# Kernel tuning notes

Hardware: AMD Instinct MI355X
Metric: run time of the kernel (lower is better)

The kernel has to match this reference:

```python
import jax, jax.numpy as jnp
import numpy as np

M, K, N = 4096, 4096, 11008

def setup_inputs() -> dict:
    key = jax.random.key(0)
    k1, k2, k3, k4 = jax.random.split(key, 4)
    x = jax.random.normal(k1, (M, K), dtype=jnp.float32)
    weight = jax.random.randint(k2, (K, N), 0, 127, dtype=jnp.int32)
    antiquant_scale = jax.random.uniform(k3, (N,), dtype=jnp.float32)
    antiquant_offset = jax.random.normal(k4, (N,), dtype=jnp.float32)
    return {"x": x, "weight": weight, "antiquant_scale": antiquant_scale, "antiquant_offset": antiquant_offset}

def reference(x, weight, antiquant_scale, antiquant_offset):
    # Dequantize: (w + offset) * scale, per output channel (broadcast over K)
    dequantized_weight = (weight.astype(jnp.float32) + antiquant_offset) * antiquant_scale  # [K, N]
    return jnp.matmul(x, dequantized_weight)  # [M, N]
```

## Files before the change

kernel.cpp:

```cpp
#include <hip/hip_runtime.h>
#include <hip/hip_bf16.h>
#include <stdint.h>

#define M_DIM 4096
#define K_DIM 4096
#define N_DIM 11008
#define BKT 64
#define NT (K_DIM / BKT)
#define GRID_MN 688
#define NBLK_M 16

typedef __attribute__((ext_vector_type(8))) short short8;
typedef __attribute__((ext_vector_type(4))) float floatx4;

__device__ __forceinline__ short f2bf(float f) {
  union { float f; uint32_t u; } c; c.f = f;
  uint32_t u = c.u;
  u += 0x7FFFu + ((u >> 16) & 1u);
  return (short)(u >> 16);
}

__device__ __forceinline__ void gload_lds16(const void* g, void* l) {
  __builtin_amdgcn_global_load_lds(
      (const __attribute__((address_space(1))) unsigned int*)g,
      (__attribute__((address_space(3))) unsigned int*)l, 16, 0, 0);
}

__global__ __launch_bounds__(256) void convert_x_kernel(const float* __restrict__ x,
                                                        short* __restrict__ xb,
                                                        float* __restrict__ rowsum) {
  const int m = blockIdx.x;
  const int t = threadIdx.x;
  const float* row = x + (size_t)m * K_DIM + t * 16;
  short* orow = xb + (size_t)m * K_DIM + t * 16;
  float4 v0 = *(const float4*)(row + 0);
  float4 v1 = *(const float4*)(row + 4);
  float4 v2 = *(const float4*)(row + 8);
  float4 v3 = *(const float4*)(row + 12);
  float sum = v0.x + v0.y + v0.z + v0.w
            + v1.x + v1.y + v1.z + v1.w
            + v2.x + v2.y + v2.z + v2.w
            + v3.x + v3.y + v3.z + v3.w;
  short8 o0, o1;
  o0[0] = f2bf(v0.x); o0[1] = f2bf(v0.y); o0[2] = f2bf(v0.z); o0[3] = f2bf(v0.w);
  o0[4] = f2bf(v1.x); o0[5] = f2bf(v1.y); o0[6] = f2bf(v1.z); o0[7] = f2bf(v1.w);
  o1[0] = f2bf(v2.x); o1[1] = f2bf(v2.y); o1[2] = f2bf(v2.z); o1[3] = f2bf(v2.w);
  o1[4] = f2bf(v3.x); o1[5] = f2bf(v3.y); o1[6] = f2bf(v3.z); o1[7] = f2bf(v3.w);
  *(short8*)(orow) = o0;
  *(short8*)(orow + 8) = o1;
  #pragma unroll
  for (int off = 32; off > 0; off >>= 1) sum += __shfl_down(sum, off);
  __shared__ float part[4];
  if ((t & 63) == 0) part[t >> 6] = sum;
  __syncthreads();
  if (t == 0) rowsum[m] = part[0] + part[1] + part[2] + part[3];
}

__global__ __launch_bounds__(256) void convert_w_kernel(const int* __restrict__ w,
                                                        short* __restrict__ wt) {
  __shared__ short tile[64][72];
  const int bk = blockIdx.x * 64;
  const int bn = blockIdx.y * 64;
  const int t = threadIdx.x;
  const int kr = t >> 2;
  const int c0 = (t & 3) * 16;
  const int* src = w + (size_t)(bk + kr) * N_DIM + bn + c0;
  int4 a = *(const int4*)(src + 0);
  int4 b = *(const int4*)(src + 4);
  int4 c = *(const int4*)(src + 8);
  int4 d = *(const int4*)(src + 12);
  short* dst = &tile[kr][c0];
  dst[0]  = f2bf((float)a.x); dst[1]  = f2bf((float)a.y);
  dst[2]  = f2bf((float)a.z); dst[3]  = f2bf((float)a.w);
  dst[4]  = f2bf((float)b.x); dst[5]  = f2bf((float)b.y);
  dst[6]  = f2bf((float)b.z); dst[7]  = f2bf((float)b.w);
  dst[8]  = f2bf((float)c.x); dst[9]  = f2bf((float)c.y);
  dst[10] = f2bf((float)c.z); dst[11] = f2bf((float)c.w);
  dst[12] = f2bf((float)d.x); dst[13] = f2bf((float)d.y);
  dst[14] = f2bf((float)d.z); dst[15] = f2bf((float)d.w);
  __syncthreads();
  const int nr = t >> 2;
  short8 o0, o1;
  #pragma unroll
  for (int j = 0; j < 8; ++j) o0[j] = tile[c0 + j][nr];
  #pragma unroll
  for (int j = 0; j < 8; ++j) o1[j] = tile[c0 + 8 + j][nr];
  short* odst = wt + (size_t)(bn + nr) * K_DIM + bk + c0;
  *(short8*)(odst) = o0;
  *(short8*)(odst + 8) = o1;
}

__global__ __launch_bounds__(512, 2) void gemm_kernel(const short* __restrict__ xb,
                                                      const short* __restrict__ wt,
                                                      const float* __restrict__ scale,
                                                      const float* __restrict__ offset,
                                                      const float* __restrict__ rowsum,
                                                      float* __restrict__ out) {
  __shared__ short lds[2][4][8192];
  const int tid = threadIdx.x;
  const int bid = blockIdx.x;
  const int wg = (bid & 7) * (GRID_MN / 8) + (bid >> 3);
  const int bm = (wg % NBLK_M) * 256;
  const int bn = (wg / NBLK_M) * 256;

  const int wid = tid >> 6;
  const int lane = tid & 63;
  const int wr = wid >> 2;
  const int wc = wid & 3;
  const int hb = wc >> 1;
  const int lr = lane & 15;
  const int lg = lane >> 4;
  const int swz = lr & 7;
  const int gk0 = (lg ^ swz) * 8;
  const int gk1 = ((lg ^ 4) ^ swz) * 8;
  const int brow = (wc & 1) * 64 + lr;

  const int srow = tid >> 3;
  const int glog = (tid & 7) ^ (srow & 7);

  const size_t toff = (size_t)srow * K_DIM + glog * 8;
  const short* pA0 = xb + (size_t)bm * K_DIM + toff;
  const short* pA1 = xb + ((size_t)bm + 128) * K_DIM + toff;
  const short* pB0 = wt + (size_t)bn * K_DIM + toff;
  const short* pB1 = wt + ((size_t)bn + 128) * K_DIM + toff;

  auto stage2 = [&](const short* p, short* region) {
    gload_lds16(p, (char*)region + tid * 16);
    gload_lds16(p + (size_t)64 * K_DIM, (char*)region + (tid + 512) * 16);
  };

  floatx4 acc[8][4];
  const floatx4 zero = {0.f, 0.f, 0.f, 0.f};
  #pragma unroll
  for (int i = 0; i < 8; ++i)
    #pragma unroll
    for (int j = 0; j < 4; ++j) acc[i][j] = zero;

  stage2(pA0, &lds[0][0][0]);
  stage2(pA1, &lds[0][1][0]);
  stage2(pB0, &lds[0][2][0]);
  stage2(pB1, &lds[0][3][0]);
  stage2(pB0 + BKT, &lds[1][2][0]);
  stage2(pA0 + BKT, &lds[1][0][0]);
  stage2(pB1 + BKT, &lds[1][3][0]);
  asm volatile("s_waitcnt vmcnt(6)" ::: "memory");
  __builtin_amdgcn_s_barrier();
  pA1 += BKT;
  pA0 += 2 * BKT;
  pB0 += 2 * BKT;
  pB1 += 2 * BKT;

  const short* const AsB[2] = {&lds[0][wr][0], &lds[1][wr][0]};
  const short* const BsB[2] = {&lds[0][2 + hb][0], &lds[1][2 + hb][0]};

  short8 a03[4][2], a47[4][2], b0[2][2], b1[2][2];
  {
    const short* As = AsB[0];
    #pragma unroll
    for (int mf = 0; mf < 4; ++mf) {
      const short* p = As + (mf * 16 + lr) * 64;
      a03[mf][0] = *(const short8*)(p + gk0);
      a03[mf][1] = *(const short8*)(p + gk1);
    }
    const short* Bsp = BsB[0];
    #pragma unroll
    for (int nf = 0; nf < 2; ++nf) {
      const short* p = Bsp + (brow + nf * 16) * 64;
      b0[nf][0] = *(const short8*)(p + gk0);
      b0[nf][1] = *(const short8*)(p + gk1);
    }
  }

#define STEP_BODY(G, GN)                                                       \
  {                                                                            \
    const short* As = AsB[G];                                                  \
    const short* Bs = BsB[G];                                                  \
                    \
    _Pragma("unroll")                                                          \
    for (int mf = 0; mf < 4; ++mf) {                                           \
      const short* p = As + ((mf + 4) * 16 + lr) * 64;                         \
      a47[mf][0] = *(const short8*)(p + gk0);                                  \
      a47[mf][1] = *(const short8*)(p + gk1);                                  \
    }                                                                          \
    asm volatile("s_waitcnt lgkmcnt(8)" ::: "memory");                         \
    __builtin_amdgcn_s_barrier();                                              \
    if (u + 1 < NT) stage2(pA1, &lds[GN][1][0]);                               \
    pA1 += BKT;                                                                \
    __builtin_amdgcn_s_setprio(1);                                             \
    _Pragma("unroll")                                                          \
    for (int mf = 0; mf < 4; ++mf)                                             \
      _Pragma("unroll")                                                        \
      for (int nf = 0; nf < 2; ++nf) {                                         \
        acc[mf][nf] = __builtin_amdgcn_mfma_f32_16x16x32_bf16(a03[mf][0], b0[nf][0], acc[mf][nf], 0, 0, 0); \
        acc[mf][nf] = __builtin_amdgcn_mfma_f32_16x16x32_bf16(a03[mf][1], b0[nf][1], acc[mf][nf], 0, 0, 0); \
      }                                                                        \
    __builtin_amdgcn_s_setprio(0);                                             \
                      \
    _Pragma("unroll")                                                          \
    for (int nf = 0; nf < 2; ++nf) {                                           \
      const short* q = Bs + (brow + (nf + 2) * 16) * 64;                       \
      b1[nf][0] = *(const short8*)(q + gk0);                                   \
      b1[nf][1] = *(const short8*)(q + gk1);                                   \
    }                                                                          \
    asm volatile("s_waitcnt lgkmcnt(4)" ::: "memory");                         \
    __builtin_amdgcn_s_barrier();                                              \
    if (u + 2 < NT) stage2(pA0, &lds[G][0][0]);                                \
    pA0 += BKT;                                                                \
    __builtin_amdgcn_s_setprio(1);                                             \
    _Pragma("unroll")                                                          \
    for (int mf = 0; mf < 4; ++mf)                                             \
      _Pragma("unroll")                                                        \
      for (int nf = 0; nf < 2; ++nf) {                                         \
        acc[mf + 4][nf] = __builtin_amdgcn_mfma_f32_16x16x32_bf16(a47[mf][0], b0[nf][0], acc[mf + 4][nf], 0, 0, 0); \
        acc[mf + 4][nf] = __builtin_amdgcn_mfma_f32_16x16x32_bf16(a47[mf][1], b0[nf][1], acc[mf + 4][nf], 0, 0, 0); \
      }                                                                        \
    __builtin_amdgcn_s_setprio(0);                                             \
                                  \
    asm volatile("s_waitcnt lgkmcnt(0)" ::: "memory");                         \
    __builtin_amdgcn_s_barrier();                                              \
    if (u + 2 < NT) stage2(pB0, &lds[G][2][0]);                                \
    pB0 += BKT;                                                                \
    __builtin_amdgcn_s_setprio(1);                                             \
    _Pragma("unroll")                                                          \
    for (int mf = 0; mf < 4; ++mf)                                             \
      _Pragma("unroll")                                                        \
      for (int nf = 0; nf < 2; ++nf) {                                         \
        acc[mf][nf + 2] = __builtin_amdgcn_mfma_f32_16x16x32_bf16(a03[mf][0], b1[nf][0], acc[mf][nf + 2], 0, 0, 0); \
        acc[mf][nf + 2] = __builtin_amdgcn_mfma_f32_16x16x32_bf16(a03[mf][1], b1[nf][1], acc[mf][nf + 2], 0, 0, 0); \
      }                                                                        \
    __builtin_amdgcn_s_setprio(0);                                             \
      \
    if (u + 2 < NT) {                                                          \
      stage2(pB1, &lds[G][3][0]);                                              \
      asm volatile("s_waitcnt vmcnt(6)" ::: "memory");                         \
    } else {                                                                   \
      asm volatile("s_waitcnt vmcnt(0)" ::: "memory");                         \
    }                                                                          \
    pB1 += BKT;                                                                \
    __builtin_amdgcn_s_barrier();                                              \
    if (u + 1 < NT) {                                                          \
      const short* An = AsB[GN];                                               \
      const short* Bn = BsB[GN];                                               \
      _Pragma("unroll")                                                        \
      for (int mf = 0; mf < 4; ++mf) {                                         \
        const short* p = An + (mf * 16 + lr) * 64;                             \
        a03[mf][0] = *(const short8*)(p + gk0);                                \
        a03[mf][1] = *(const short8*)(p + gk1);                                \
      }                                                                        \
      _Pragma("unroll")                                                        \
      for (int nf = 0; nf < 2; ++nf) {                                         \
        const short* p = Bn + (brow + nf * 16) * 64;                           \
        b0[nf][0] = *(const short8*)(p + gk0);                                 \
        b0[nf][1] = *(const short8*)(p + gk1);                                 \
      }                                                                        \
    }                                                                          \
    __builtin_amdgcn_s_setprio(1);                                             \
    _Pragma("unroll")                                                          \
    for (int mf = 0; mf < 4; ++mf)                                             \
      _Pragma("unroll")                                                        \
      for (int nf = 0; nf < 2; ++nf) {                                         \
        acc[mf + 4][nf + 2] = __builtin_amdgcn_mfma_f32_16x16x32_bf16(a47[mf][0], b1[nf][0], acc[mf + 4][nf + 2], 0, 0, 0); \
        acc[mf + 4][nf + 2] = __builtin_amdgcn_mfma_f32_16x16x32_bf16(a47[mf][1], b1[nf][1], acc[mf + 4][nf + 2], 0, 0, 0); \
      }                                                                        \
    __builtin_amdgcn_s_setprio(0);                                             \
  }

  for (int u = 0; u < NT; u += 2) {
    STEP_BODY(0, 1)
    ++u;
    STEP_BODY(1, 0)
    --u;
  }
#undef STEP_BODY

  const int orow0 = bm + wr * 128 + lg * 4;
  const int ocol0 = bn + wc * 64 + lr;
  float4 rsv[8];
  #pragma unroll
  for (int amf = 0; amf < 8; ++amf)
    rsv[amf] = *(const float4*)&rowsum[orow0 + amf * 16];
  #pragma unroll
  for (int anf = 0; anf < 4; ++anf) {
    const int n = ocol0 + anf * 16;
    const float sc = scale[n];
    const float of = offset[n];
    #pragma unroll
    for (int amf = 0; amf < 8; ++amf) {
      const int mbase = orow0 + amf * 16;
      const float4 rv = rsv[amf];
      out[(size_t)(mbase + 0) * N_DIM + n] = (acc[amf][anf][0] + of * rv.x) * sc;
      out[(size_t)(mbase + 1) * N_DIM + n] = (acc[amf][anf][1] + of * rv.y) * sc;
      out[(size_t)(mbase + 2) * N_DIM + n] = (acc[amf][anf][2] + of * rv.z) * sc;
      out[(size_t)(mbase + 3) * N_DIM + n] = (acc[amf][anf][3] + of * rv.w) * sc;
    }
  }
}

__global__ __launch_bounds__(256) void fallback_gemm(const float* __restrict__ x,
                                                     const int* __restrict__ w,
                                                     const float* __restrict__ scale,
                                                     const float* __restrict__ offset,
                                                     float* __restrict__ out) {
  __shared__ float xs[32][33];
  __shared__ float bs[32][33];
  const int bm = blockIdx.y * 32, bn = blockIdx.x * 32;
  const int t = threadIdx.x;
  const int tm = t >> 5, tn = t & 31;
  float acc[4] = {0.f, 0.f, 0.f, 0.f};
  for (int k0 = 0; k0 < K_DIM; k0 += 32) {
    #pragma unroll
    for (int i = 0; i < 4; ++i) {
      int idx = t + i * 256; int r = idx >> 5, c = idx & 31;
      xs[r][c] = x[(size_t)(bm + r) * K_DIM + k0 + c];
      bs[r][c] = ((float)w[(size_t)(k0 + r) * N_DIM + bn + c] + offset[bn + c]) * scale[bn + c];
    }
    __syncthreads();
    #pragma unroll 8
    for (int kk = 0; kk < 32; ++kk) {
      float wv = bs[kk][tn];
      #pragma unroll
      for (int i = 0; i < 4; ++i) acc[i] += xs[tm + 8 * i][kk] * wv;
    }
    __syncthreads();
  }
  #pragma unroll
  for (int i = 0; i < 4; ++i)
    out[(size_t)(bm + tm + 8 * i) * N_DIM + bn + tn] = acc[i];
}

extern "C" void kernel_launch(void* const* d_in, const int* in_sizes, int n_in,
                              void* d_out, int out_size, void* d_ws, size_t ws_size,
                              hipStream_t stream) {
  const float* x      = (const float*)d_in[0];
  const int*   w      = (const int*)d_in[1];
  const float* scale  = (const float*)d_in[2];
  const float* offset = (const float*)d_in[3];
  float* out = (float*)d_out;

  const size_t xb_bytes = (size_t)M_DIM * K_DIM * 2;
  const size_t wt_bytes = (size_t)N_DIM * K_DIM * 2;
  const size_t rs_bytes = (size_t)M_DIM * 4;

  if (ws_size >= xb_bytes + wt_bytes + rs_bytes) {
    short* xb = (short*)d_ws;
    short* wt = (short*)((char*)d_ws + xb_bytes);
    float* rowsum = (float*)((char*)d_ws + xb_bytes + wt_bytes);
    convert_x_kernel<<<M_DIM, 256, 0, stream>>>(x, xb, rowsum);
    convert_w_kernel<<<dim3(K_DIM / 64, N_DIM / 64), 256, 0, stream>>>(w, wt);
    gemm_kernel<<<GRID_MN, 512, 0, stream>>>(xb, wt, scale, offset, rowsum, out);
  } else {
    fallback_gemm<<<dim3(N_DIM / 32, M_DIM / 32), 256, 0, stream>>>(x, w, scale, offset, out);
  }
}
```

Baseline: 405.6 us.

## Pre-swizzle weights into MFMA fragment layout and load B directly to registers

The weight conversion kernel now writes bf16 weights in a fragment-ordered layout of 16-column by 32-k tiles, so each lane can load its MFMA B operands straight from global memory into registers. The GEMM drops the LDS staging for B, halving shared memory use, and restructures the K loop with fewer barriers, explicit vmcnt/lgkmcnt waits and a peeled tail. This removes LDS traffic and barrier overhead for B. In exchange it relies on register-level global loads being latency-hidden, and B tiles are no longer shared across waves through LDS, which raises global and L2 traffic.

```diff
diff --git a/kernel.cpp b/kernel.cpp
--- a/kernel.cpp
+++ b/kernel.cpp
@@ -12,6 +12,8 @@
 
 typedef __attribute__((ext_vector_type(8))) short short8;
 typedef __attribute__((ext_vector_type(4))) float floatx4;
+
+#define MFMA16 __builtin_amdgcn_mfma_f32_16x16x32_bf16
 
 __device__ __forceinline__ short f2bf(float f) {
   union { float f; uint32_t u; } c; c.f = f;
@@ -57,7 +59,7 @@
 }
 
 __global__ __launch_bounds__(256) void convert_w_kernel(const int* __restrict__ w,
-                                                        short* __restrict__ wt) {
+                                                        short* __restrict__ wt2) {
   __shared__ short tile[64][72];
   const int bk = blockIdx.x * 64;
   const int bn = blockIdx.y * 64;
@@ -79,24 +81,38 @@
   dst[12] = f2bf((float)d.x); dst[13] = f2bf((float)d.y);
   dst[14] = f2bf((float)d.z); dst[15] = f2bf((float)d.w);
   __syncthreads();
-  const int nr = t >> 2;
+  const int blk = t >> 5;
+  const int ktN_l = blk & 1;
+  const int nt_l = blk >> 1;
   short8 o0, o1;
-  #pragma unroll
-  for (int j = 0; j < 8; ++j) o0[j] = tile[c0 + j][nr];
-  #pragma unroll
-  for (int j = 0; j < 8; ++j) o1[j] = tile[c0 + 8 + j][nr];
-  short* odst = wt + (size_t)(bn + nr) * K_DIM + bk + c0;
-  *(short8*)(odst) = o0;
-  *(short8*)(odst + 8) = o1;
+  {
+    const int l = (t & 31) * 2;
+    const int nl = nt_l * 16 + (l & 15);
+    const int kb = ktN_l * 32 + (l >> 4) * 8;
+    #pragma unroll
+    for (int j = 0; j < 8; ++j) o0[j] = tile[kb + j][nl];
+  }
+  {
+    const int l = (t & 31) * 2 + 1;
+    const int nl = nt_l * 16 + (l & 15);
+    const int kb = ktN_l * 32 + (l >> 4) * 8;
+    #pragma unroll
+    for (int j = 0; j < 8; ++j) o1[j] = tile[kb + j][nl];
+  }
+  const size_t nt_g = (size_t)(bn >> 4) + nt_l;
+  const size_t ktN_g = (size_t)(bk >> 5) + ktN_l;
+  short* od = wt2 + (nt_g * 128 + ktN_g) * 512 + (size_t)((t & 31) * 2) * 8;
+  *(short8*)(od) = o0;
+  *(short8*)(od + 8) = o1;
 }
 
 __global__ __launch_bounds__(512, 2) void gemm_kernel(const short* __restrict__ xb,
-                                                      const short* __restrict__ wt,
+                                                      const short* __restrict__ wt2,
                                                       const float* __restrict__ scale,
                                                       const float* __restrict__ offset,
                                                       const float* __restrict__ rowsum,
                                                       float* __restrict__ out) {
-  __shared__ short lds[2][4][8192];
+  __shared__ short lds[2][2][8192];
   const int tid = threadIdx.x;
   const int bid = blockIdx.x;
   const int wg = (bid & 7) * (GRID_MN / 8) + (bid >> 3);
@@ -107,28 +123,29 @@
   const int lane = tid & 63;
   const int wr = wid >> 2;
   const int wc = wid & 3;
-  const int hb = wc >> 1;
   const int lr = lane & 15;
   const int lg = lane >> 4;
   const int swz = lr & 7;
   const int gk0 = (lg ^ swz) * 8;
   const int gk1 = ((lg ^ 4) ^ swz) * 8;
-  const int brow = (wc & 1) * 64 + lr;
 
   const int srow = tid >> 3;
   const int glog = (tid & 7) ^ (srow & 7);
-
   const size_t toff = (size_t)srow * K_DIM + glog * 8;
   const short* pA0 = xb + (size_t)bm * K_DIM + toff;
   const short* pA1 = xb + ((size_t)bm + 128) * K_DIM + toff;
-  const short* pB0 = wt + (size_t)bn * K_DIM + toff;
-  const short* pB1 = wt + ((size_t)bn + 128) * K_DIM + toff;
 
   auto stage2 = [&](const short* p, short* region) {
     gload_lds16(p, (char*)region + tid * 16);
     gload_lds16(p + (size_t)64 * K_DIM, (char*)region + (tid + 512) * 16);
   };
 
+  const int ntb = (bn >> 4) + wc * 4;
+  const short* bp0 = wt2 + (size_t)(ntb + 0) * 65536 + (size_t)lane * 8;
+  const short* bp1 = wt2 + (size_t)(ntb + 1) * 65536 + (size_t)lane * 8;
+  const short* bp2 = wt2 + (size_t)(ntb + 2) * 65536 + (size_t)lane * 8;
+  const short* bp3 = wt2 + (size_t)(ntb + 3) * 65536 + (size_t)lane * 8;
+
   floatx4 acc[8][4];
   const floatx4 zero = {0.f, 0.f, 0.f, 0.f};
   #pragma unroll
@@ -136,24 +153,22 @@
     #pragma unroll
     for (int j = 0; j < 4; ++j) acc[i][j] = zero;
 
+  short8 a03[4][2], a47[4][2], b0[2][2], b1[2][2];
+
   stage2(pA0, &lds[0][0][0]);
   stage2(pA1, &lds[0][1][0]);
-  stage2(pB0, &lds[0][2][0]);
-  stage2(pB1, &lds[0][3][0]);
-  stage2(pB0 + BKT, &lds[1][2][0]);
+  b0[0][0] = *(const short8*)(bp0); b0[0][1] = *(const short8*)(bp0 + 512);
+  b0[1][0] = *(const short8*)(bp1); b0[1][1] = *(const short8*)(bp1 + 512);
   stage2(pA0 + BKT, &lds[1][0][0]);
-  stage2(pB1 + BKT, &lds[1][3][0]);
-  asm volatile("s_waitcnt vmcnt(6)" ::: "memory");
+  b1[0][0] = *(const short8*)(bp2); b1[0][1] = *(const short8*)(bp2 + 512);
+  b1[1][0] = *(const short8*)(bp3); b1[1][1] = *(const short8*)(bp3 + 512);
+  bp0 += 1024; bp1 += 1024; bp2 += 1024; bp3 += 1024;
+  pA0 += 2 * BKT;
+  pA1 += BKT;
+  asm volatile("s_waitcnt vmcnt(10)" ::: "memory");
   __builtin_amdgcn_s_barrier();
-  pA1 += BKT;
-  pA0 += 2 * BKT;
-  pB0 += 2 * BKT;
-  pB1 += 2 * BKT;
 
   const short* const AsB[2] = {&lds[0][wr][0], &lds[1][wr][0]};
-  const short* const BsB[2] = {&lds[0][2 + hb][0], &lds[1][2 + hb][0]};
-
-  short8 a03[4][2], a47[4][2], b0[2][2], b1[2][2];
   {
     const short* As = AsB[0];
     #pragma unroll
@@ -162,116 +177,96 @@
       a03[mf][0] = *(const short8*)(p + gk0);
       a03[mf][1] = *(const short8*)(p + gk1);
     }
-    const short* Bsp = BsB[0];
-    #pragma unroll
-    for (int nf = 0; nf < 2; ++nf) {
-      const short* p = Bsp + (brow + nf * 16) * 64;
-      b0[nf][0] = *(const short8*)(p + gk0);
-      b0[nf][1] = *(const short8*)(p + gk1);
-    }
-  }
-
-#define STEP_BODY(G, GN)                                                       \
+  }
+
+#define STEP(G, GN, A0STG, TAILF)                                              \
   {                                                                            \
     const short* As = AsB[G];                                                  \
-    const short* Bs = BsB[G];                                                  \
-                    \
+                                                             \
+    asm volatile("s_waitcnt lgkmcnt(0)" ::: "memory");                         \
+    if (TAILF) { asm volatile("s_waitcnt vmcnt(4)" ::: "memory"); }            \
+    else       { asm volatile("s_waitcnt vmcnt(6)" ::: "memory"); }            \
+    __builtin_amdgcn_sched_barrier(0);                                         \
     _Pragma("unroll")                                                          \
     for (int mf = 0; mf < 4; ++mf) {                                           \
       const short* p = As + ((mf + 4) * 16 + lr) * 64;                         \
       a47[mf][0] = *(const short8*)(p + gk0);                                  \
       a47[mf][1] = *(const short8*)(p + gk1);                                  \
     }                                                                          \
-    asm volatile("s_waitcnt lgkmcnt(8)" ::: "memory");                         \
-    __builtin_amdgcn_s_barrier();                                              \
-    if (u + 1 < NT) stage2(pA1, &lds[GN][1][0]);                               \
-    pA1 += BKT;                                                                \
+    if (!TAILF) { stage2(pA1, &lds[GN][1][0]); pA1 += BKT; }                   \
     __builtin_amdgcn_s_setprio(1);                                             \
     _Pragma("unroll")                                                          \
     for (int mf = 0; mf < 4; ++mf)                                             \
       _Pragma("unroll")                                                        \
       for (int nf = 0; nf < 2; ++nf) {                                         \
-        acc[mf][nf] = __builtin_amdgcn_mfma_f32_16x16x32_bf16(a03[mf][0], b0[nf][0], acc[mf][nf], 0, 0, 0); \
-        acc[mf][nf] = __builtin_amdgcn_mfma_f32_16x16x32_bf16(a03[mf][1], b0[nf][1], acc[mf][nf], 0, 0, 0); \
+        acc[mf][nf] = MFMA16(a03[mf][0], b0[nf][0], acc[mf][nf], 0, 0, 0);     \
+        acc[mf][nf] = MFMA16(a03[mf][1], b0[nf][1], acc[mf][nf], 0, 0, 0);     \
       }                                                                        \
     __builtin_amdgcn_s_setprio(0);                                             \
-                      \
-    _Pragma("unroll")                                                          \
-    for (int nf = 0; nf < 2; ++nf) {                                           \
-      const short* q = Bs + (brow + (nf + 2) * 16) * 64;                       \
-      b1[nf][0] = *(const short8*)(q + gk0);                                   \
-      b1[nf][1] = *(const short8*)(q + gk1);                                   \
+                                                             \
+    asm volatile("s_waitcnt lgkmcnt(0)" ::: "memory");                         \
+    __builtin_amdgcn_sched_barrier(0);                                         \
+    __builtin_amdgcn_s_setprio(1);                                             \
+    _Pragma("unroll")                                                          \
+    for (int mf = 0; mf < 4; ++mf)                                             \
+      _Pragma("unroll")                                                        \
+      for (int nf = 0; nf < 2; ++nf) {                                         \
+        acc[mf + 4][nf] = MFMA16(a47[mf][0], b0[nf][0], acc[mf + 4][nf], 0, 0, 0); \
+        acc[mf + 4][nf] = MFMA16(a47[mf][1], b0[nf][1], acc[mf + 4][nf], 0, 0, 0); \
+      }                                                                        \
+    __builtin_amdgcn_s_setprio(0);                                             \
+    if (!TAILF) {                                                              \
+      b0[0][0] = *(const short8*)(bp0); b0[0][1] = *(const short8*)(bp0 + 512);\
+      b0[1][0] = *(const short8*)(bp1); b0[1][1] = *(const short8*)(bp1 + 512);\
     }                                                                          \
-    asm volatile("s_waitcnt lgkmcnt(4)" ::: "memory");                         \
-    __builtin_amdgcn_s_barrier();                                              \
-    if (u + 2 < NT) stage2(pA0, &lds[G][0][0]);                                \
-    pA0 += BKT;                                                                \
+                                                             \
+    if (TAILF) { asm volatile("s_waitcnt vmcnt(0)" ::: "memory"); }            \
+    else       { asm volatile("s_waitcnt vmcnt(6)" ::: "memory"); }            \
+    __builtin_amdgcn_sched_barrier(0);                                         \
     __builtin_amdgcn_s_setprio(1);                                             \
     _Pragma("unroll")                                                          \
     for (int mf = 0; mf < 4; ++mf)                                             \
       _Pragma("unroll")                                                        \
       for (int nf = 0; nf < 2; ++nf) {                                         \
-        acc[mf + 4][nf] = __builtin_amdgcn_mfma_f32_16x16x32_bf16(a47[mf][0], b0[nf][0], acc[mf + 4][nf], 0, 0, 0); \
-        acc[mf + 4][nf] = __builtin_amdgcn_mfma_f32_16x16x32_bf16(a47[mf][1], b0[nf][1], acc[mf + 4][nf], 0, 0, 0); \
+        acc[mf + 4][nf + 2] = MFMA16(a47[mf][0], b1[nf][0], acc[mf + 4][nf + 2], 0, 0, 0); \
+        acc[mf + 4][nf + 2] = MFMA16(a47[mf][1], b1[nf][1], acc[mf + 4][nf + 2], 0, 0, 0); \
       }                                                                        \
     __builtin_amdgcn_s_setprio(0);                                             \
-                                  \
-    asm volatile("s_waitcnt lgkmcnt(0)" ::: "memory");                         \
-    __builtin_amdgcn_s_barrier();                                              \
-    if (u + 2 < NT) stage2(pB0, &lds[G][2][0]);                                \
-    pB0 += BKT;                                                                \
+                                                             \
+    if (TAILF) { asm volatile("s_waitcnt vmcnt(0)" ::: "memory"); }            \
+    else       { asm volatile("s_waitcnt vmcnt(4)" ::: "memory"); }            \
+    if (!TAILF) __builtin_amdgcn_s_barrier();                                  \
+    if (A0STG) { stage2(pA0, &lds[G][0][0]); pA0 += BKT; }                     \
     __builtin_amdgcn_s_setprio(1);                                             \
     _Pragma("unroll")                                                          \
     for (int mf = 0; mf < 4; ++mf)                                             \
       _Pragma("unroll")                                                        \
       for (int nf = 0; nf < 2; ++nf) {                                         \
-        acc[mf][nf + 2] = __builtin_amdgcn_mfma_f32_16x16x32_bf16(a03[mf][0], b1[nf][0], acc[mf][nf + 2], 0, 0, 0); \
-        acc[mf][nf + 2] = __builtin_amdgcn_mfma_f32_16x16x32_bf16(a03[mf][1], b1[nf][1], acc[mf][nf + 2], 0, 0, 0); \
+        acc[mf][nf + 2] = MFMA16(a03[mf][0], b1[nf][0], acc[mf][nf + 2], 0, 0, 0); \
+        acc[mf][nf + 2] = MFMA16(a03[mf][1], b1[nf][1], acc[mf][nf + 2], 0, 0, 0); \
       }                                                                        \
     __builtin_amdgcn_s_setprio(0);                                             \
-      \
-    if (u + 2 < NT) {                                                          \
-      stage2(pB1, &lds[G][3][0]);                                              \
-      asm volatile("s_waitcnt vmcnt(6)" ::: "memory");                         \
-    } else {                                                                   \
-      asm volatile("s_waitcnt vmcnt(0)" ::: "memory");                         \
-    }                                                                          \
-    pB1 += BKT;                                                                \
-    __builtin_amdgcn_s_barrier();                                              \
-    if (u + 1 < NT) {                                                          \
+    if (!TAILF) {                                                              \
+      b1[0][0] = *(const short8*)(bp2); b1[0][1] = *(const short8*)(bp2 + 512);\
+      b1[1][0] = *(const short8*)(bp3); b1[1][1] = *(const short8*)(bp3 + 512);\
+      bp0 += 1024; bp1 += 1024; bp2 += 1024; bp3 += 1024;                      \
       const short* An = AsB[GN];                                               \
-      const short* Bn = BsB[GN];                                               \
       _Pragma("unroll")                                                        \
       for (int mf = 0; mf < 4; ++mf) {                                         \
         const short* p = An + (mf * 16 + lr) * 64;                             \
         a03[mf][0] = *(const short8*)(p + gk0);                                \
         a03[mf][1] = *(const short8*)(p + gk1);                                \
       }                                                                        \
-      _Pragma("unroll")                                                        \
-      for (int nf = 0; nf < 2; ++nf) {                                         \
-        const short* p = Bn + (brow + nf * 16) * 64;                           \
-        b0[nf][0] = *(const short8*)(p + gk0);                                 \
-        b0[nf][1] = *(const short8*)(p + gk1);                                 \
-      }                                                                        \
     }                                                                          \
-    __builtin_amdgcn_s_setprio(1);                                             \
-    _Pragma("unroll")                                                          \
-    for (int mf = 0; mf < 4; ++mf)                                             \
-      _Pragma("unroll")                                                        \
-      for (int nf = 0; nf < 2; ++nf) {                                         \
-        acc[mf + 4][nf + 2] = __builtin_amdgcn_mfma_f32_16x16x32_bf16(a47[mf][0], b1[nf][0], acc[mf + 4][nf + 2], 0, 0, 0); \
-        acc[mf + 4][nf + 2] = __builtin_amdgcn_mfma_f32_16x16x32_bf16(a47[mf][1], b1[nf][1], acc[mf + 4][nf + 2], 0, 0, 0); \
-      }                                                                        \
-    __builtin_amdgcn_s_setprio(0);                                             \
-  }
-
-  for (int u = 0; u < NT; u += 2) {
-    STEP_BODY(0, 1)
-    ++u;
-    STEP_BODY(1, 0)
-    --u;
-  }
-#undef STEP_BODY
+  }
+
+  for (int u = 0; u < NT - 2; u += 2) {
+    STEP(0, 1, 1, 0)
+    STEP(1, 0, 1, 0)
+  }
+  STEP(0, 1, 0, 0)
+  STEP(1, 0, 0, 1)
+#undef STEP
 
   const int orow0 = bm + wr * 128 + lg * 4;
   const int ocol0 = bn + wc * 64 + lr;
@@ -343,11 +338,11 @@
 
   if (ws_size >= xb_bytes + wt_bytes + rs_bytes) {
     short* xb = (short*)d_ws;
-    short* wt = (short*)((char*)d_ws + xb_bytes);
+    short* wt2 = (short*)((char*)d_ws + xb_bytes);
     float* rowsum = (float*)((char*)d_ws + xb_bytes + wt_bytes);
     convert_x_kernel<<<M_DIM, 256, 0, stream>>>(x, xb, rowsum);
-    convert_w_kernel<<<dim3(K_DIM / 64, N_DIM / 64), 256, 0, stream>>>(w, wt);
-    gemm_kernel<<<GRID_MN, 512, 0, stream>>>(xb, wt, scale, offset, rowsum, out);
+    convert_w_kernel<<<dim3(K_DIM / 64, N_DIM / 64), 256, 0, stream>>>(w, wt2);
+    gemm_kernel<<<GRID_MN, 512, 0, stream>>>(xb, wt2, scale, offset, rowsum, out);
   } else {
     fallback_gemm<<<dim3(N_DIM / 32, M_DIM / 32), 256, 0, stream>>>(x, w, scale, offset, out);
   }
```

Result: slower. 476.4 us (+17.5%).
